# Kernel optimization log

Hardware: AMD Instinct MI355X
Metric: run time of the kernel (lower is better)

## Reference

```python
import jax, jax.numpy as jnp
import numpy as np

N_NODES = 50000
N_EDGES = 800000
IN_DIM = 256
HID_DIM = 128   # 2 * output_dim
OUT_DIM = 64


def setup_inputs() -> dict:
    key = jax.random.key(0)
    ks = jax.random.split(key, 6)
    x = jax.random.normal(ks[0], (N_NODES, IN_DIM), dtype=jnp.float32)
    edge_index = jax.random.randint(ks[1], (2, N_EDGES), 0, N_NODES, dtype=jnp.int32)
    W1 = jax.random.normal(ks[2], (IN_DIM, HID_DIM), dtype=jnp.float32) * (1.0 / np.sqrt(IN_DIM))
    b1 = jnp.zeros((HID_DIM,), dtype=jnp.float32)
    W2 = jax.random.normal(ks[3], (HID_DIM, OUT_DIM), dtype=jnp.float32) * (1.0 / np.sqrt(HID_DIM))
    b2 = jnp.zeros((OUT_DIM,), dtype=jnp.float32)
    return {"x": x, "edge_index": edge_index, "W1": W1, "b1": b1, "W2": W2, "b2": b2}


def _gcn_layer(h, src, dst, norm, W, b, n):
    # linear transform then normalized scatter-add aggregation (GCNConv)
    h = h @ W                                   # [N, F_out]
    msg = h[src] * norm[:, None]                # gather + per-edge normalization
    agg = jax.ops.segment_sum(msg, dst, num_segments=n)
    return agg + b


def reference(x, edge_index, W1, b1, W2, b2):
    n = x.shape[0]
    loops = jnp.arange(n, dtype=edge_index.dtype)
    src = jnp.concatenate([edge_index[0], loops])   # add self-loops (GCNConv default)
    dst = jnp.concatenate([edge_index[1], loops])
    # symmetric normalization deg^-1/2[src] * deg^-1/2[dst], deg incl. self-loops
    deg = jax.ops.segment_sum(jnp.ones_like(dst, dtype=x.dtype), dst, num_segments=n)
    dinv = jnp.where(deg > 0, jax.lax.rsqrt(jnp.maximum(deg, 1.0)), 0.0)
    norm = dinv[src] * dinv[dst]
    h = jax.nn.relu(_gcn_layer(x, src, dst, norm, W1, b1, n))
    return _gcn_layer(h, src, dst, norm, W2, b2, n)
```

## Files before the change

### kernel.cpp

```cpp
#include <hip/hip_runtime.h>

#define NN 50000
#define NE 800000
#define IND 256
#define HD 128
#define OD 64
#define SCAN_NBLK ((NN + 1023) / 1024)
#define DEG_BLKS ((NE + 255) / 256)
#define G1_BLKS ((NN + 63) / 64)

typedef __attribute__((ext_vector_type(8))) short short8;
typedef __attribute__((ext_vector_type(4))) float f32x4;
typedef __attribute__((ext_vector_type(4))) uint u32x4;

static __device__ __forceinline__ ushort f2bf(float f) {
    uint u = __float_as_uint(f);
    u += 0x7fff + ((u >> 16) & 1);
    return (ushort)(u >> 16);
}
static __device__ __forceinline__ float bf2f(ushort h) {
    return __uint_as_float(((uint)h) << 16);
}

template<int N, int K>
static __device__ __forceinline__ void prep_w_body(const float* __restrict__ W,
                                                   uint* __restrict__ Wp, int i) {
    constexpr int NT = N / 16;
    constexpr int TOT = (K / 32) * NT * 256;
    if (i >= TOT) return;
    int region = i >> 8;
    int lane = (i >> 2) & 63;
    int jp = i & 3;
    int c8 = region / NT, nt = region % NT;
    int k = c8 * 32 + (lane >> 4) * 8 + jp * 2;
    int n = nt * 16 + (lane & 15);
    Wp[i] = (uint)f2bf(W[k * N + n]) | ((uint)f2bf(W[(k + 1) * N + n]) << 16);
}

__global__ void degrank_prep_k(const int* __restrict__ dst, int* __restrict__ deg,
                               int* __restrict__ rank,
                               const float* __restrict__ W1, uint* __restrict__ W1p,
                               const float* __restrict__ W2, uint* __restrict__ W2p) {
    int b = blockIdx.x;
    if (b < DEG_BLKS) {
        int e = b * 256 + threadIdx.x;
        if (e < NE) rank[e] = atomicAdd(&deg[dst[e]], 1);
    } else if (b < DEG_BLKS + 64) {
        prep_w_body<HD, IND>(W1, W1p, (b - DEG_BLKS) * 256 + threadIdx.x);
    } else {
        prep_w_body<OD, HD>(W2, W2p, (b - DEG_BLKS - 64) * 256 + threadIdx.x);
    }
}


__launch_bounds__(1024)
__global__ void scan1_k(const int* __restrict__ deg, int* __restrict__ off,
                        int* __restrict__ btot, float* __restrict__ dinv) {
    __shared__ int wsum[16];
    const int tid = threadIdx.x, lane = tid & 63, wv = tid >> 6;
    const int idx = blockIdx.x * 1024 + tid;
    int v = (idx < NN) ? deg[idx] : 0;
    if (idx < NN) dinv[idx] = rsqrtf((float)v + 1.0f);
    int inc = v;
#pragma unroll
    for (int ofs = 1; ofs < 64; ofs <<= 1) {
        int t = __shfl_up(inc, ofs, 64);
        if (lane >= ofs) inc += t;
    }
    if (lane == 63) wsum[wv] = inc;
    __syncthreads();
    int wprefix = 0;
#pragma unroll
    for (int w = 0; w < 16; ++w) wprefix += (w < wv) ? wsum[w] : 0;
    if (idx < NN) off[idx] = wprefix + inc - v;
    if (tid == 1023) btot[blockIdx.x] = wprefix + inc;
}

__launch_bounds__(64)
__global__ void scan2_k(int* __restrict__ btot, int* __restrict__ off) {
    const int lane = threadIdx.x;
    int v = (lane < SCAN_NBLK) ? btot[lane] : 0;
    int inc = v;
#pragma unroll
    for (int ofs = 1; ofs < 64; ofs <<= 1) {
        int t = __shfl_up(inc, ofs, 64);
        if (lane >= ofs) inc += t;
    }
    if (lane < SCAN_NBLK) btot[lane] = inc - v;
    if (lane == 63) off[NN] = inc;
}

__launch_bounds__(1024)
__global__ void scan3_k(int* __restrict__ off, const int* __restrict__ btot) {
    const int idx = blockIdx.x * 1024 + threadIdx.x;
    if (idx < NN) off[idx] += btot[blockIdx.x];
}

__launch_bounds__(256)
__global__ void gemm1_fill_k(const float* __restrict__ x, const uint* __restrict__ Wp,
                             const float* __restrict__ rs, ushort* __restrict__ Cbf,
                             const int* __restrict__ src, const int* __restrict__ dst,
                             const int* __restrict__ off, const int* __restrict__ rank,
                             int* __restrict__ csr) {
    constexpr int N = HD, K = IND;
    constexpr int NT = N / 16;
    constexpr int KH = K / 128;
    constexpr int NREG = 4 * NT;
    __shared__ uint bsl[NREG * 256];

    if (blockIdx.x >= G1_BLKS) {
        int e = (int)(blockIdx.x - G1_BLKS) * 256 + threadIdx.x;
        if (e < NE) {
            int d = dst[e];
            csr[off[d] + rank[e]] = src[e];
        }
        return;
    }

    const int tid = threadIdx.x, lane = tid & 63, wv = tid >> 6;
    const int row = blockIdx.x * 64 + wv * 16 + (lane & 15);
    const int rowc = min(row, NN - 1);
    const int kl = (lane >> 4) * 8;

    f32x4 acc[NT];
#pragma unroll
    for (int t = 0; t < NT; ++t) acc[t] = (f32x4){0.f, 0.f, 0.f, 0.f};

    for (int h = 0; h < KH; ++h) {
        if (h) __syncthreads();
#pragma unroll
        for (int rg = wv; rg < NREG; rg += 4)
            __builtin_amdgcn_global_load_lds(
                (const uint __attribute__((address_space(1)))*)(Wp + (size_t)(h * NREG + rg) * 256 + lane * 4),
                (uint __attribute__((address_space(3)))*)&bsl[rg * 256], 16, 0, 0);
        __syncthreads();
#pragma unroll
        for (int c = 0; c < 4; ++c) {
            const int k0 = h * 128 + c * 32;
            f32x4 lo = *(const f32x4*)&x[(size_t)rowc * K + k0 + kl];
            f32x4 hi = *(const f32x4*)&x[(size_t)rowc * K + k0 + kl + 4];
            short8 af;
            af[0] = (short)f2bf(lo.x); af[1] = (short)f2bf(lo.y);
            af[2] = (short)f2bf(lo.z); af[3] = (short)f2bf(lo.w);
            af[4] = (short)f2bf(hi.x); af[5] = (short)f2bf(hi.y);
            af[6] = (short)f2bf(hi.z); af[7] = (short)f2bf(hi.w);
#pragma unroll
            for (int t = 0; t < NT; ++t) {
                short8 bf = *(const short8*)&bsl[(c * NT + t) * 256 + lane * 4];
                acc[t] = __builtin_amdgcn_mfma_f32_16x16x32_bf16(af, bf, acc[t], 0, 0, 0);
            }
        }
    }
    const int crow = blockIdx.x * 64 + wv * 16 + (lane >> 4) * 4;
#pragma unroll
    for (int t = 0; t < NT; ++t) {
        int col = t * 16 + (lane & 15);
#pragma unroll
        for (int r = 0; r < 4; ++r)
            if (crow + r < NN)
                Cbf[(size_t)(crow + r) * N + col] = f2bf(acc[t][r] * rs[crow + r]);
    }
}

template<int N, int K>
__launch_bounds__(256)
__global__ void mfma_gemm_k(const ushort* __restrict__ Ap, const uint* __restrict__ Wp,
                            const float* __restrict__ rs, ushort* __restrict__ Cbf,
                            int M) {
    constexpr int NT = N / 16;
    constexpr int KH = K / 128;
    constexpr int NREG = 4 * NT;
    __shared__ uint bsl[NREG * 256];
    const int tid = threadIdx.x, lane = tid & 63, wv = tid >> 6;
    const int row = blockIdx.x * 64 + wv * 16 + (lane & 15);
    const int rowc = min(row, M - 1);
    const int kl = (lane >> 4) * 8;

    f32x4 acc[NT];
#pragma unroll
    for (int t = 0; t < NT; ++t) acc[t] = (f32x4){0.f, 0.f, 0.f, 0.f};

    for (int h = 0; h < KH; ++h) {
        if (h) __syncthreads();
#pragma unroll
        for (int rg = wv; rg < NREG; rg += 4)
            __builtin_amdgcn_global_load_lds(
                (const uint __attribute__((address_space(1)))*)(Wp + (size_t)(h * NREG + rg) * 256 + lane * 4),
                (uint __attribute__((address_space(3)))*)&bsl[rg * 256], 16, 0, 0);
        __syncthreads();
#pragma unroll
        for (int c = 0; c < 4; ++c) {
            const int k0 = h * 128 + c * 32;
            short8 af = *(const short8*)&Ap[(size_t)rowc * K + k0 + kl];
#pragma unroll
            for (int t = 0; t < NT; ++t) {
                short8 bf = *(const short8*)&bsl[(c * NT + t) * 256 + lane * 4];
                acc[t] = __builtin_amdgcn_mfma_f32_16x16x32_bf16(af, bf, acc[t], 0, 0, 0);
            }
        }
    }
    const int crow = blockIdx.x * 64 + wv * 16 + (lane >> 4) * 4;
#pragma unroll
    for (int t = 0; t < NT; ++t) {
        int col = t * 16 + (lane & 15);
#pragma unroll
        for (int r = 0; r < 4; ++r)
            if (crow + r < M)
                Cbf[(size_t)(crow + r) * N + col] = f2bf(acc[t][r] * rs[crow + r]);
    }
}


__launch_bounds__(256)
__global__ void gather1_k(const ushort* __restrict__ feat, const int* __restrict__ csr,
                          const int* __restrict__ off, const float* __restrict__ dinv,
                          const float* __restrict__ bias, ushort* __restrict__ outbf) {
    const int w = (int)((blockIdx.x * 256 + threadIdx.x) >> 6);
    const int lane = threadIdx.x & 63;
    if (w >= NN) return;
    const int g = lane >> 4;
    const int c = lane & 15;
    const int o0 = off[w], o1 = off[w + 1];

    float a[8];
    if (g == 0) {
        u32x4 sv = *(const u32x4*)&feat[(size_t)w * HD + c * 8];
#pragma unroll
        for (int j = 0; j < 4; ++j) {
            a[2 * j]     = bf2f((ushort)sv[j]);
            a[2 * j + 1] = bf2f((ushort)(sv[j] >> 16));
        }
    } else {
#pragma unroll
        for (int j = 0; j < 8; ++j) a[j] = 0.f;
    }
    for (int i = o0; i < o1; i += 4) {
        int idx = i + g;
        if (idx < o1) {
            int s = csr[idx];
            u32x4 v = *(const u32x4*)&feat[(size_t)s * HD + c * 8];
#pragma unroll
            for (int j = 0; j < 4; ++j) {
                a[2 * j]     += bf2f((ushort)v[j]);
                a[2 * j + 1] += bf2f((ushort)(v[j] >> 16));
            }
        }
    }
#pragma unroll
    for (int j = 0; j < 8; ++j) {
        a[j] += __shfl_xor(a[j], 16, 64);
        a[j] += __shfl_xor(a[j], 32, 64);
    }
    if (g == 0) {
        float dd = dinv[w];
        u32x4 o;
#pragma unroll
        for (int j = 0; j < 4; ++j) {
            float r0 = fmaxf(fmaf(a[2 * j],     dd, bias[c * 8 + 2 * j]),     0.f);
            float r1 = fmaxf(fmaf(a[2 * j + 1], dd, bias[c * 8 + 2 * j + 1]), 0.f);
            o[j] = (uint)f2bf(r0) | ((uint)f2bf(r1) << 16);
        }
        *(u32x4*)&outbf[(size_t)w * HD + c * 8] = o;
    }
}

__launch_bounds__(256)
__global__ void gather2_k(const ushort* __restrict__ feat, const int* __restrict__ csr,
                          const int* __restrict__ off, const float* __restrict__ dinv,
                          const float* __restrict__ bias, float* __restrict__ out) {
    const int w = (int)((blockIdx.x * 256 + threadIdx.x) >> 6);
    const int lane = threadIdx.x & 63;
    if (w >= NN) return;
    const int g = lane >> 3;
    const int c = lane & 7;
    const int o0 = off[w], o1 = off[w + 1];

    float a[8];
    if (g == 0) {
        u32x4 sv = *(const u32x4*)&feat[(size_t)w * OD + c * 8];
#pragma unroll
        for (int j = 0; j < 4; ++j) {
            a[2 * j]     = bf2f((ushort)sv[j]);
            a[2 * j + 1] = bf2f((ushort)(sv[j] >> 16));
        }
    } else {
#pragma unroll
        for (int j = 0; j < 8; ++j) a[j] = 0.f;
    }
    for (int i = o0; i < o1; i += 8) {
        int idx = i + g;
        if (idx < o1) {
            int s = csr[idx];
            u32x4 v = *(const u32x4*)&feat[(size_t)s * OD + c * 8];
#pragma unroll
            for (int j = 0; j < 4; ++j) {
                a[2 * j]     += bf2f((ushort)v[j]);
                a[2 * j + 1] += bf2f((ushort)(v[j] >> 16));
            }
        }
    }
#pragma unroll
    for (int j = 0; j < 8; ++j) {
        a[j] += __shfl_xor(a[j], 8, 64);
        a[j] += __shfl_xor(a[j], 16, 64);
        a[j] += __shfl_xor(a[j], 32, 64);
    }
    if (g == 0) {
        float dd = dinv[w];
        float4 lo, hi;
        lo.x = fmaf(a[0], dd, bias[c * 8 + 0]);
        lo.y = fmaf(a[1], dd, bias[c * 8 + 1]);
        lo.z = fmaf(a[2], dd, bias[c * 8 + 2]);
        lo.w = fmaf(a[3], dd, bias[c * 8 + 3]);
        hi.x = fmaf(a[4], dd, bias[c * 8 + 4]);
        hi.y = fmaf(a[5], dd, bias[c * 8 + 5]);
        hi.z = fmaf(a[6], dd, bias[c * 8 + 6]);
        hi.w = fmaf(a[7], dd, bias[c * 8 + 7]);
        *(float4*)&out[(size_t)w * OD + c * 8]     = lo;
        *(float4*)&out[(size_t)w * OD + c * 8 + 4] = hi;
    }
}

extern "C" void kernel_launch(void* const* d_in, const int* in_sizes, int n_in,
                              void* d_out, int out_size, void* d_ws, size_t ws_size,
                              hipStream_t stream) {
    const float* x   = (const float*)d_in[0];
    const int*   src = (const int*)d_in[1];
    const int*   dst = ((const int*)d_in[1]) + NE;
    const float* W1  = (const float*)d_in[2];
    const float* b1  = (const float*)d_in[3];
    const float* W2  = (const float*)d_in[4];
    const float* b2  = (const float*)d_in[5];
    float* out = (float*)d_out;

    float*  dinv   = (float*)d_ws;
    uint*   W1p    = (uint*)(dinv + 50048);
    uint*   W2p    = W1p + 16384;
    ushort* h1s_bf = (ushort*)(W2p + 4096);
    ushort* h_bf   = h1s_bf + (size_t)NN * HD;
    ushort* gs_bf  = h_bf + (size_t)NN * HD;
    int* deg_i  = (int*)(gs_bf + (size_t)NN * OD);
    int* off    = deg_i + 50048;
    int* rank   = off + 50052;
    int* btot   = rank + NE;
    int* csr    = btot + 64;

    hipMemsetAsync(deg_i, 0, 50048 * sizeof(int), stream);
    degrank_prep_k<<<DEG_BLKS + 64 + 16, 256, 0, stream>>>(dst, deg_i, rank,
                                                           W1, W1p, W2, W2p);
    scan1_k<<<SCAN_NBLK, 1024, 0, stream>>>(deg_i, off, btot, dinv);
    scan2_k<<<1, 64, 0, stream>>>(btot, off);
    scan3_k<<<SCAN_NBLK, 1024, 0, stream>>>(off, btot);

    gemm1_fill_k<<<G1_BLKS + DEG_BLKS, 256, 0, stream>>>(x, W1p, dinv, h1s_bf,
                                                         src, dst, off, rank, csr);
    gather1_k<<<(NN + 3) / 4, 256, 0, stream>>>(h1s_bf, csr, off, dinv, b1, h_bf);

    mfma_gemm_k<OD, HD><<<(NN + 63) / 64, 256, 0, stream>>>(h_bf, W2p, dinv, gs_bf, NN);
    gather2_k<<<(NN + 3) / 4, 256, 0, stream>>>(gs_bf, csr, off, dinv, b2, out);
}
```

Baseline: 235.7 us.

## Fuse degree atomics into GEMM1, fold scan fixup into CSR fill, use 16-bit indices

The degree and rank atomics now run in the same launch as the first GEMM. That GEMM no longer scales rows by dinv, so it no longer has to wait for the scan. Instead, gather1 applies dinv[dst] to the self term and dinv[src] per edge. The third scan pass is folded into the CSR fill kernel, which also writes a corrected offset array. Rank and CSR source indices are stored as 16-bit values to cut index traffic in the gathers, which only works because node count and degrees stay below 65536. The cost is an extra random dinv load per edge in gather1.

```diff
diff --git a/kernel.cpp b/kernel.cpp
--- a/kernel.cpp
+++ b/kernel.cpp
@@ -8,6 +8,7 @@
 #define SCAN_NBLK ((NN + 1023) / 1024)
 #define DEG_BLKS ((NE + 255) / 256)
 #define G1_BLKS ((NN + 63) / 64)
+#define FIN_BLKS ((NN + 256) / 256)
 
 typedef __attribute__((ext_vector_type(8))) short short8;
 typedef __attribute__((ext_vector_type(4))) float f32x4;
@@ -37,18 +38,72 @@
     Wp[i] = (uint)f2bf(W[k * N + n]) | ((uint)f2bf(W[(k + 1) * N + n]) << 16);
 }
 
-__global__ void degrank_prep_k(const int* __restrict__ dst, int* __restrict__ deg,
-                               int* __restrict__ rank,
-                               const float* __restrict__ W1, uint* __restrict__ W1p,
-                               const float* __restrict__ W2, uint* __restrict__ W2p) {
+__global__ void prep_k(const float* __restrict__ W1, uint* __restrict__ W1p,
+                       const float* __restrict__ W2, uint* __restrict__ W2p) {
     int b = blockIdx.x;
-    if (b < DEG_BLKS) {
-        int e = b * 256 + threadIdx.x;
-        if (e < NE) rank[e] = atomicAdd(&deg[dst[e]], 1);
-    } else if (b < DEG_BLKS + 64) {
-        prep_w_body<HD, IND>(W1, W1p, (b - DEG_BLKS) * 256 + threadIdx.x);
-    } else {
-        prep_w_body<OD, HD>(W2, W2p, (b - DEG_BLKS - 64) * 256 + threadIdx.x);
+    if (b < 64) prep_w_body<HD, IND>(W1, W1p, b * 256 + threadIdx.x);
+    else        prep_w_body<OD, HD>(W2, W2p, (b - 64) * 256 + threadIdx.x);
+}
+
+__launch_bounds__(256)
+__global__ void mega_k(const float* __restrict__ x, const uint* __restrict__ Wp,
+                       ushort* __restrict__ Cbf,
+                       const int* __restrict__ dst, int* __restrict__ deg,
+                       ushort* __restrict__ rank) {
+    constexpr int N = HD, K = IND;
+    constexpr int NT = N / 16;
+    constexpr int KH = K / 128;
+    constexpr int NREG = 4 * NT;
+    __shared__ uint bsl[NREG * 256];
+
+    if (blockIdx.x >= G1_BLKS) {
+        int e = (int)(blockIdx.x - G1_BLKS) * 256 + threadIdx.x;
+        if (e < NE) rank[e] = (ushort)atomicAdd(&deg[dst[e]], 1);
+        return;
+    }
+
+    const int tid = threadIdx.x, lane = tid & 63, wv = tid >> 6;
+    const int row = blockIdx.x * 64 + wv * 16 + (lane & 15);
+    const int rowc = min(row, NN - 1);
+    const int kl = (lane >> 4) * 8;
+
+    f32x4 acc[NT];
+#pragma unroll
+    for (int t = 0; t < NT; ++t) acc[t] = (f32x4){0.f, 0.f, 0.f, 0.f};
+
+    for (int h = 0; h < KH; ++h) {
+        if (h) __syncthreads();
+#pragma unroll
+        for (int rg = wv; rg < NREG; rg += 4)
+            __builtin_amdgcn_global_load_lds(
+                (const uint __attribute__((address_space(1)))*)(Wp + (size_t)(h * NREG + rg) * 256 + lane * 4),
+                (uint __attribute__((address_space(3)))*)&bsl[rg * 256], 16, 0, 0);
+        __syncthreads();
+#pragma unroll
+        for (int c = 0; c < 4; ++c) {
+            const int k0 = h * 128 + c * 32;
+            f32x4 lo = *(const f32x4*)&x[(size_t)rowc * K + k0 + kl];
+            f32x4 hi = *(const f32x4*)&x[(size_t)rowc * K + k0 + kl + 4];
+            short8 af;
+            af[0] = (short)f2bf(lo.x); af[1] = (short)f2bf(lo.y);
+            af[2] = (short)f2bf(lo.z); af[3] = (short)f2bf(lo.w);
+            af[4] = (short)f2bf(hi.x); af[5] = (short)f2bf(hi.y);
+            af[6] = (short)f2bf(hi.z); af[7] = (short)f2bf(hi.w);
+#pragma unroll
+            for (int t = 0; t < NT; ++t) {
+                short8 bf = *(const short8*)&bsl[(c * NT + t) * 256 + lane * 4];
+                acc[t] = __builtin_amdgcn_mfma_f32_16x16x32_bf16(af, bf, acc[t], 0, 0, 0);
+            }
+        }
+    }
+    const int crow = blockIdx.x * 64 + wv * 16 + (lane >> 4) * 4;
+#pragma unroll
+    for (int t = 0; t < NT; ++t) {
+        int col = t * 16 + (lane & 15);
+#pragma unroll
+        for (int r = 0; r < 4; ++r)
+            if (crow + r < NN)
+                Cbf[(size_t)(crow + r) * N + col] = f2bf(acc[t][r]);
     }
 }
 
@@ -90,75 +145,22 @@
     if (lane == 63) off[NN] = inc;
 }
 
-__launch_bounds__(1024)
-__global__ void scan3_k(int* __restrict__ off, const int* __restrict__ btot) {
-    const int idx = blockIdx.x * 1024 + threadIdx.x;
-    if (idx < NN) off[idx] += btot[blockIdx.x];
-}
-
-__launch_bounds__(256)
-__global__ void gemm1_fill_k(const float* __restrict__ x, const uint* __restrict__ Wp,
-                             const float* __restrict__ rs, ushort* __restrict__ Cbf,
-                             const int* __restrict__ src, const int* __restrict__ dst,
-                             const int* __restrict__ off, const int* __restrict__ rank,
-                             int* __restrict__ csr) {
-    constexpr int N = HD, K = IND;
-    constexpr int NT = N / 16;
-    constexpr int KH = K / 128;
-    constexpr int NREG = 4 * NT;
-    __shared__ uint bsl[NREG * 256];
-
-    if (blockIdx.x >= G1_BLKS) {
-        int e = (int)(blockIdx.x - G1_BLKS) * 256 + threadIdx.x;
+__global__ void fillf_k(const int* __restrict__ src, const int* __restrict__ dst,
+                        const int* __restrict__ off, const int* __restrict__ btot,
+                        const ushort* __restrict__ rank, ushort* __restrict__ csr,
+                        int* __restrict__ off2) {
+    int b = blockIdx.x;
+    if (b < DEG_BLKS) {
+        int e = b * 256 + threadIdx.x;
         if (e < NE) {
             int d = dst[e];
-            csr[off[d] + rank[e]] = src[e];
-        }
-        return;
-    }
-
-    const int tid = threadIdx.x, lane = tid & 63, wv = tid >> 6;
-    const int row = blockIdx.x * 64 + wv * 16 + (lane & 15);
-    const int rowc = min(row, NN - 1);
-    const int kl = (lane >> 4) * 8;
-
-    f32x4 acc[NT];
-#pragma unroll
-    for (int t = 0; t < NT; ++t) acc[t] = (f32x4){0.f, 0.f, 0.f, 0.f};
-
-    for (int h = 0; h < KH; ++h) {
-        if (h) __syncthreads();
-#pragma unroll
-        for (int rg = wv; rg < NREG; rg += 4)
-            __builtin_amdgcn_global_load_lds(
-                (const uint __attribute__((address_space(1)))*)(Wp + (size_t)(h * NREG + rg) * 256 + lane * 4),
-                (uint __attribute__((address_space(3)))*)&bsl[rg * 256], 16, 0, 0);
-        __syncthreads();
-#pragma unroll
-        for (int c = 0; c < 4; ++c) {
-            const int k0 = h * 128 + c * 32;
-            f32x4 lo = *(const f32x4*)&x[(size_t)rowc * K + k0 + kl];
-            f32x4 hi = *(const f32x4*)&x[(size_t)rowc * K + k0 + kl + 4];
-            short8 af;
-            af[0] = (short)f2bf(lo.x); af[1] = (short)f2bf(lo.y);
-            af[2] = (short)f2bf(lo.z); af[3] = (short)f2bf(lo.w);
-            af[4] = (short)f2bf(hi.x); af[5] = (short)f2bf(hi.y);
-            af[6] = (short)f2bf(hi.z); af[7] = (short)f2bf(hi.w);
-#pragma unroll
-            for (int t = 0; t < NT; ++t) {
-                short8 bf = *(const short8*)&bsl[(c * NT + t) * 256 + lane * 4];
-                acc[t] = __builtin_amdgcn_mfma_f32_16x16x32_bf16(af, bf, acc[t], 0, 0, 0);
-            }
-        }
-    }
-    const int crow = blockIdx.x * 64 + wv * 16 + (lane >> 4) * 4;
-#pragma unroll
-    for (int t = 0; t < NT; ++t) {
-        int col = t * 16 + (lane & 15);
-#pragma unroll
-        for (int r = 0; r < 4; ++r)
-            if (crow + r < NN)
-                Cbf[(size_t)(crow + r) * N + col] = f2bf(acc[t][r] * rs[crow + r]);
+            int o = off[d] + btot[d >> 10];
+            csr[o + rank[e]] = (ushort)src[e];
+        }
+    } else {
+        int idx = (b - DEG_BLKS) * 256 + threadIdx.x;
+        if (idx < NN) off2[idx] = off[idx] + btot[idx >> 10];
+        else if (idx == NN) off2[NN] = off[NN];
     }
 }
 
@@ -210,9 +212,8 @@
     }
 }
 
-
 __launch_bounds__(256)
-__global__ void gather1_k(const ushort* __restrict__ feat, const int* __restrict__ csr,
+__global__ void gather1_k(const ushort* __restrict__ feat, const ushort* __restrict__ csr,
                           const int* __restrict__ off, const float* __restrict__ dinv,
                           const float* __restrict__ bias, ushort* __restrict__ outbf) {
     const int w = (int)((blockIdx.x * 256 + threadIdx.x) >> 6);
@@ -221,14 +222,15 @@
     const int g = lane >> 4;
     const int c = lane & 15;
     const int o0 = off[w], o1 = off[w + 1];
+    const float dd = dinv[w];
 
     float a[8];
     if (g == 0) {
         u32x4 sv = *(const u32x4*)&feat[(size_t)w * HD + c * 8];
 #pragma unroll
         for (int j = 0; j < 4; ++j) {
-            a[2 * j]     = bf2f((ushort)sv[j]);
-            a[2 * j + 1] = bf2f((ushort)(sv[j] >> 16));
+            a[2 * j]     = bf2f((ushort)sv[j]) * dd;
+            a[2 * j + 1] = bf2f((ushort)(sv[j] >> 16)) * dd;
         }
     } else {
 #pragma unroll
@@ -238,11 +240,12 @@
         int idx = i + g;
         if (idx < o1) {
             int s = csr[idx];
+            float ds = dinv[s];
             u32x4 v = *(const u32x4*)&feat[(size_t)s * HD + c * 8];
 #pragma unroll
             for (int j = 0; j < 4; ++j) {
-                a[2 * j]     += bf2f((ushort)v[j]);
-                a[2 * j + 1] += bf2f((ushort)(v[j] >> 16));
+                a[2 * j]     = fmaf(bf2f((ushort)v[j]),         ds, a[2 * j]);
+                a[2 * j + 1] = fmaf(bf2f((ushort)(v[j] >> 16)), ds, a[2 * j + 1]);
             }
         }
     }
@@ -252,7 +255,6 @@
         a[j] += __shfl_xor(a[j], 32, 64);
     }
     if (g == 0) {
-        float dd = dinv[w];
         u32x4 o;
 #pragma unroll
         for (int j = 0; j < 4; ++j) {
@@ -265,7 +267,7 @@
 }
 
 __launch_bounds__(256)
-__global__ void gather2_k(const ushort* __restrict__ feat, const int* __restrict__ csr,
+__global__ void gather2_k(const ushort* __restrict__ feat, const ushort* __restrict__ csr,
                           const int* __restrict__ off, const float* __restrict__ dinv,
                           const float* __restrict__ bias, float* __restrict__ out) {
     const int w = (int)((blockIdx.x * 256 + threadIdx.x) >> 6);
@@ -336,26 +338,28 @@
     float*  dinv   = (float*)d_ws;
     uint*   W1p    = (uint*)(dinv + 50048);
     uint*   W2p    = W1p + 16384;
-    ushort* h1s_bf = (ushort*)(W2p + 4096);
-    ushort* h_bf   = h1s_bf + (size_t)NN * HD;
+    ushort* h1u_bf = (ushort*)(W2p + 4096);
+    ushort* h_bf   = h1u_bf + (size_t)NN * HD;
     ushort* gs_bf  = h_bf + (size_t)NN * HD;
     int* deg_i  = (int*)(gs_bf + (size_t)NN * OD);
     int* off    = deg_i + 50048;
-    int* rank   = off + 50052;
-    int* btot   = rank + NE;
-    int* csr    = btot + 64;
+    int* off2   = off + 50052;
+    int* btot   = off2 + 50052;
+    ushort* rank = (ushort*)(btot + 64);
+    ushort* csr  = rank + NE;
 
     hipMemsetAsync(deg_i, 0, 50048 * sizeof(int), stream);
-    degrank_prep_k<<<DEG_BLKS + 64 + 16, 256, 0, stream>>>(dst, deg_i, rank,
-                                                           W1, W1p, W2, W2p);
+    prep_k<<<80, 256, 0, stream>>>(W1, W1p, W2, W2p);
+
+    mega_k<<<G1_BLKS + DEG_BLKS, 256, 0, stream>>>(x, W1p, h1u_bf, dst, deg_i, rank);
+
     scan1_k<<<SCAN_NBLK, 1024, 0, stream>>>(deg_i, off, btot, dinv);
     scan2_k<<<1, 64, 0, stream>>>(btot, off);
-    scan3_k<<<SCAN_NBLK, 1024, 0, stream>>>(off, btot);
-
-    gemm1_fill_k<<<G1_BLKS + DEG_BLKS, 256, 0, stream>>>(x, W1p, dinv, h1s_bf,
-                                                         src, dst, off, rank, csr);
-    gather1_k<<<(NN + 3) / 4, 256, 0, stream>>>(h1s_bf, csr, off, dinv, b1, h_bf);
+
+    fillf_k<<<DEG_BLKS + FIN_BLKS, 256, 0, stream>>>(src, dst, off, btot, rank, csr, off2);
+
+    gather1_k<<<(NN + 3) / 4, 256, 0, stream>>>(h1u_bf, csr, off2, dinv, b1, h_bf);
 
     mfma_gemm_k<OD, HD><<<(NN + 63) / 64, 256, 0, stream>>>(h_bf, W2p, dinv, gs_bf, NN);
-    gather2_k<<<(NN + 3) / 4, 256, 0, stream>>>(gs_bf, csr, off, dinv, b2, out);
-}
+    gather2_k<<<(NN + 3) / 4, 256, 0, stream>>>(gs_bf, csr, off2, dinv, b2, out);
+}
```

Result: faster. 217.2 us (-7.8%).
